# Performance work log

Measured on AMD Instinct MI355X. Metric: run time of the kernel, lower is better.

## Reference

```python
import jax, jax.numpy as jnp
import numpy as np

DIN = 128
HID = 128
B, N = 32, 2048
NEG = 9000000000000000.0


def setup_inputs() -> dict:
    key = jax.random.key(0)
    ks = jax.random.split(key, 8)
    x = jax.random.normal(ks[0], (B, N, DIN), dtype=jnp.float32)
    mask = jax.random.randint(ks[1], (B, N, N), 0, 2).astype(jnp.float32)
    s = 1.0 / np.sqrt(DIN)
    Wv = jax.random.uniform(ks[2], (DIN, HID), minval=-s, maxval=s, dtype=jnp.float32)
    bv = jax.random.uniform(ks[3], (HID,), minval=-s, maxval=s, dtype=jnp.float32)
    Wk = jax.random.uniform(ks[4], (DIN, HID), minval=-s, maxval=s, dtype=jnp.float32)
    bk = jax.random.uniform(ks[5], (HID,), minval=-s, maxval=s, dtype=jnp.float32)
    Wq = jax.random.uniform(ks[6], (DIN, HID), minval=-s, maxval=s, dtype=jnp.float32)
    bq = jax.random.uniform(ks[7], (HID,), minval=-s, maxval=s, dtype=jnp.float32)
    return {"x": x, "mask": mask, "Wv": Wv, "bv": bv, "Wk": Wk, "bk": bk, "Wq": Wq, "bq": bq}


def reference(x, mask, Wv, bv, Wk, bk, Wq, bq):
    v = jnp.tanh(x @ Wv + bv)            # [B, N, H]
    q = jnp.tanh(x @ Wq + bq)            # [B, N, H]
    k = jnp.tanh(x @ Wk + bk)            # [B, N, H]
    scores = jnp.einsum('bih,bjh->bij', q, k)  # [B, N, N]
    scores = scores * mask - NEG * (1.0 - mask)
    att = jax.nn.softmax(scores, axis=-1)
    out = jnp.einsum('bij,bjh->bih', att, v)   # [B, N, H]
    return out
```

## Files before the change

kernel.cpp:

```cpp
#include <hip/hip_runtime.h>

#define DIN 128
#define HID 128
#define BB  32
#define NN  2048
#define LOG2E 1.44269504088896340736f
#define PROJ_BLOCKS 1024
#define COMP_BLOCKS 32768

typedef float  f32x4   __attribute__((ext_vector_type(4)));
typedef __bf16 bf16x4v __attribute__((ext_vector_type(4)));
typedef __bf16 bf16x8  __attribute__((ext_vector_type(8)));

__device__ __forceinline__ float tanh_fast(float x) {
  float e = __expf(2.0f * x);
  return 1.0f - 2.0f / (e + 1.0f);
}

__global__ __launch_bounds__(256) void wt_kernel(
    const float* __restrict__ Wq, const float* __restrict__ Wk,
    const float* __restrict__ Wv, __bf16* __restrict__ wt) {
  const float* W = (blockIdx.x == 0) ? Wq : (blockIdx.x == 1) ? Wk : Wv;
  __bf16* dst = wt + blockIdx.x * (DIN * HID);
  int t = threadIdx.x;
#pragma unroll
  for (int c = 0; c < 16; ++c) {
    int o = c * 1024 + t * 4;
    int d = o >> 7, h = o & 127;
    f32x4 v = *(const f32x4*)(W + d * HID + h);
    dst[(h + 0) * DIN + d] = (__bf16)v.x;
    dst[(h + 1) * DIN + d] = (__bf16)v.y;
    dst[(h + 2) * DIN + d] = (__bf16)v.z;
    dst[(h + 3) * DIN + d] = (__bf16)v.w;
  }
}

__global__ __launch_bounds__(256) void proj_kernel(
    const float* __restrict__ x, const __bf16* __restrict__ wt,
    const float* __restrict__ bq, const float* __restrict__ bk,
    const float* __restrict__ bv, const float* __restrict__ mask,
    __bf16* __restrict__ qbf, __bf16* __restrict__ kbf,
    __bf16* __restrict__ vtbf, unsigned short* __restrict__ bits) {
  const int tid = threadIdx.x;

  if (blockIdx.x >= PROJ_BLOCKS) {
    const long cidx = (long)(blockIdx.x - PROJ_BLOCKS) * 256 + tid;
    const int quad = (int)(cidx & 3);
    const int jt = (int)((cidx >> 2) & 31);
    const long grow = cidx >> 7;
    const float* mp = mask + grow * NN + jt * 64 + quad * 4;
    float mb = 0.f;
#pragma unroll
    for (int t = 0; t < 4; ++t) {
      f32x4 mr = *(const f32x4*)(mp + t * 16);
#pragma unroll
      for (int r = 0; r < 4; ++r)
        mb = fmaf(mr[r], (float)(1u << (t * 4 + r)), mb);
    }
    bits[cidx] = (unsigned short)(unsigned)mb;
    return;
  }

  int lane = tid & 63, w = tid >> 6;
  int l15 = lane & 15, quad = lane >> 4;
  long i0 = (long)blockIdx.x * 64;

  bf16x8 bx[4][4];
#pragma unroll
  for (int nt = 0; nt < 4; ++nt) {
    const float* xp = x + (i0 + nt * 16 + l15) * DIN;
#pragma unroll
    for (int ks = 0; ks < 4; ++ks) {
      int d0 = ks * 32 + quad * 8;
      f32x4 a = *(const f32x4*)(xp + d0);
      f32x4 b = *(const f32x4*)(xp + d0 + 4);
      bf16x8 f;
      f[0] = (__bf16)a.x; f[1] = (__bf16)a.y; f[2] = (__bf16)a.z; f[3] = (__bf16)a.w;
      f[4] = (__bf16)b.x; f[5] = (__bf16)b.y; f[6] = (__bf16)b.z; f[7] = (__bf16)b.w;
      bx[nt][ks] = f;
    }
  }

#pragma unroll
  for (int p = 0; p < 2; ++p) {
    const __bf16* wtp = wt + p * DIN * HID;
    const float* bias = (p == 0) ? bq : bk;
    __bf16* outp = (p == 0) ? qbf : kbf;
#pragma unroll
    for (int nt = 0; nt < 8; ++nt) {
      int h0 = nt * 16 + l15;
      f32x4 acc = {0.f, 0.f, 0.f, 0.f};
#pragma unroll
      for (int ks = 0; ks < 4; ++ks) {
        bf16x8 wf = *(const bf16x8*)(wtp + (long)h0 * DIN + ks * 32 + quad * 8);
        acc = __builtin_amdgcn_mfma_f32_16x16x32_bf16(bx[w][ks], wf, acc, 0, 0, 0);
      }
      float bcol = bias[h0];
      long rowb = i0 + w * 16 + quad * 4;
#pragma unroll
      for (int r = 0; r < 4; ++r) {
        float val = tanh_fast(acc[r] + bcol);
        if (p == 0) val *= LOG2E;
        outp[(rowb + r) * HID + h0] = (__bf16)val;
      }
    }
  }

  {
    const __bf16* wtp = wt + 2 * DIN * HID;
    long bb = i0 >> 11;
    int nloc = (int)(i0 & 2047);
    long vbase = bb * (long)HID * NN;
#pragma unroll
    for (int s = 0; s < 2; ++s) {
      int hb = w * 32 + s * 16;
      bf16x8 af[4];
#pragma unroll
      for (int ks = 0; ks < 4; ++ks)
        af[ks] = *(const bf16x8*)(wtp + (long)(hb + l15) * DIN + ks * 32 + quad * 8);
      float bvr[4];
#pragma unroll
      for (int r = 0; r < 4; ++r) bvr[r] = bv[hb + quad * 4 + r];
#pragma unroll
      for (int nt = 0; nt < 4; ++nt) {
        f32x4 acc = {0.f, 0.f, 0.f, 0.f};
#pragma unroll
        for (int ks = 0; ks < 4; ++ks)
          acc = __builtin_amdgcn_mfma_f32_16x16x32_bf16(af[ks], bx[nt][ks], acc, 0, 0, 0);
        int hrow = hb + quad * 4;
        int ncol = nloc + nt * 16 + l15;
#pragma unroll
        for (int r = 0; r < 4; ++r) {
          float val = tanh_fast(acc[r] + bvr[r]);
          vtbf[vbase + (long)(hrow + r) * NN + ncol] = (__bf16)val;
        }
      }
    }
  }
}

#define KSTR 136
#define VSTR 72
#define PSTR 72

__global__ __launch_bounds__(512, 4) void attn_kernel(
    const __bf16* __restrict__ qbf, const __bf16* __restrict__ kbf,
    const __bf16* __restrict__ vtbf, const unsigned short* __restrict__ bits,
    float* __restrict__ out) {
  __shared__ __bf16 Ks[64 * KSTR];
  __shared__ __bf16 Vts[128 * VSTR];
  __shared__ __bf16 Pl[8 * 16 * PSTR];

  const int tid = threadIdx.x;
  const int lane = tid & 63, w = tid >> 6;
  const int l15 = lane & 15, quad = lane >> 4;
  const int bid = blockIdx.x;
  const int vb = (bid >> 3) | ((bid & 7) << 6);
  const int b = vb >> 4;
  const int i0 = (vb & 15) * 128;
  const long kvbase = (long)b * NN * HID;

  bf16x8 qf[4];
  {
    const __bf16* qp =
        qbf + kvbase + (long)(i0 + w * 16 + l15) * HID + quad * 8;
#pragma unroll
    for (int ks = 0; ks < 4; ++ks) qf[ks] = *(const bf16x8*)(qp + ks * 32);
  }

  const int krow = tid >> 4, kcol = (tid & 15) * 8;
  const int vrow = tid >> 3, vcol = (tid & 7) * 8;
  const __bf16* kg = kbf + kvbase + (long)krow * HID + kcol;
  const __bf16* vg = vtbf + (long)b * HID * NN + (long)vrow * NN + vcol;
  __bf16* ksd0 = Ks + krow * KSTR + kcol;
  __bf16* ksd1 = Ks + (krow + 32) * KSTR + kcol;
  __bf16* vsd0 = Vts + vrow * VSTR + vcol;
  __bf16* vsd1 = Vts + (vrow + 64) * VSTR + vcol;
  const unsigned short* bitp =
      bits + ((long)b * NN + (i0 + w * 16 + l15)) * 128 + quad;
  __bf16* Pw = Pl + w * 16 * PSTR;

  f32x4 O[8];
#pragma unroll
  for (int i = 0; i < 8; ++i) O[i] = (f32x4){0.f, 0.f, 0.f, 0.f};
  float mrow = -1e30f, lrow = 0.0f;

  bf16x8 kr0 = *(const bf16x8*)(kg);
  bf16x8 kr1 = *(const bf16x8*)(kg + 32 * HID);
  bf16x8 vr0 = *(const bf16x8*)(vg);
  bf16x8 vr1 = *(const bf16x8*)(vg + (long)64 * NN);
  unsigned mcur = bitp[0];
  *(bf16x8*)ksd0 = kr0; *(bf16x8*)ksd1 = kr1;
  *(bf16x8*)vsd0 = vr0; *(bf16x8*)vsd1 = vr1;
  __syncthreads();

#pragma unroll 1
  for (int jt = 0; jt < 32; ++jt) {
    const int jn = (jt < 31) ? jt + 1 : 31;
    {
      const __bf16* kgn = kg + (long)jn * 64 * HID;
      kr0 = *(const bf16x8*)(kgn);
      kr1 = *(const bf16x8*)(kgn + 32 * HID);
      const __bf16* vgn = vg + jn * 64;
      vr0 = *(const bf16x8*)(vgn);
      vr1 = *(const bf16x8*)(vgn + (long)64 * NN);
    }
    const unsigned mnext = bitp[jn * 4];

    f32x4 S[4];
#pragma unroll
    for (int t = 0; t < 4; ++t) {
      f32x4 acc = {0.f, 0.f, 0.f, 0.f};
      const __bf16* kp = Ks + (t * 16 + l15) * KSTR + quad * 8;
#pragma unroll
      for (int ks = 0; ks < 4; ++ks) {
        bf16x8 kf = *(const bf16x8*)(kp + ks * 32);
        acc = __builtin_amdgcn_mfma_f32_16x16x32_bf16(kf, qf[ks], acc, 0, 0, 0);
      }
      S[t] = acc;
    }

    float tmx = -1e30f;
#pragma unroll
    for (int t = 0; t < 4; ++t)
#pragma unroll
      for (int r = 0; r < 4; ++r) {
        float s = ((mcur >> (t * 4 + r)) & 1u) ? S[t][r] : -1e30f;
        S[t][r] = s;
        tmx = fmaxf(tmx, s);
      }
    tmx = fmaxf(tmx, __shfl_xor(tmx, 16));
    tmx = fmaxf(tmx, __shfl_xor(tmx, 32));
    const float mnew = fmaxf(mrow, tmx);
    const float alpha = exp2f(mrow - mnew);
    float rs = 0.0f;
#pragma unroll
    for (int t = 0; t < 4; ++t) {
      bf16x4v pb;
#pragma unroll
      for (int r = 0; r < 4; ++r) {
        float p = exp2f(S[t][r] - mnew);
        rs += p;
        pb[r] = (__bf16)p;
      }
      *(bf16x4v*)(Pw + l15 * PSTR + t * 16 + quad * 4) = pb;
    }
    rs += __shfl_xor(rs, 16);
    rs += __shfl_xor(rs, 32);
    lrow = lrow * alpha + rs;
    mrow = mnew;

    float ar[4];
#pragma unroll
    for (int r = 0; r < 4; ++r) ar[r] = __shfl(alpha, (quad << 2) + r);
#pragma unroll
    for (int nt = 0; nt < 8; ++nt)
#pragma unroll
      for (int r = 0; r < 4; ++r) O[nt][r] *= ar[r];

    const bf16x8 pf0 = *(const bf16x8*)(Pw + l15 * PSTR + quad * 8);
    const bf16x8 pf1 = *(const bf16x8*)(Pw + l15 * PSTR + 32 + quad * 8);

#pragma unroll
    for (int nt = 0; nt < 8; ++nt) {
      const __bf16* vp = Vts + (nt * 16 + l15) * VSTR + quad * 8;
      bf16x8 vf0 = *(const bf16x8*)(vp);
      bf16x8 vf1 = *(const bf16x8*)(vp + 32);
      O[nt] = __builtin_amdgcn_mfma_f32_16x16x32_bf16(pf0, vf0, O[nt], 0, 0, 0);
      O[nt] = __builtin_amdgcn_mfma_f32_16x16x32_bf16(pf1, vf1, O[nt], 0, 0, 0);
    }

    __syncthreads();
    *(bf16x8*)ksd0 = kr0; *(bf16x8*)ksd1 = kr1;
    *(bf16x8*)vsd0 = vr0; *(bf16x8*)vsd1 = vr1;
    mcur = mnext;
    __syncthreads();
  }

  const float inv = 1.0f / lrow;
  float il[4];
#pragma unroll
  for (int r = 0; r < 4; ++r) il[r] = __shfl(inv, (quad << 2) + r);
  const long rowb = (long)b * NN + i0 + w * 16 + quad * 4;
#pragma unroll
  for (int r = 0; r < 4; ++r) {
    float* op = out + (rowb + r) * HID;
#pragma unroll
    for (int nt = 0; nt < 8; ++nt) op[nt * 16 + l15] = O[nt][r] * il[r];
  }
}

extern "C" void kernel_launch(void* const* d_in, const int* in_sizes, int n_in,
                              void* d_out, int out_size, void* d_ws, size_t ws_size,
                              hipStream_t stream) {
  const float* x    = (const float*)d_in[0];
  const float* mask = (const float*)d_in[1];
  const float* Wv   = (const float*)d_in[2];
  const float* bv   = (const float*)d_in[3];
  const float* Wk   = (const float*)d_in[4];
  const float* bk   = (const float*)d_in[5];
  const float* Wq   = (const float*)d_in[6];
  const float* bq   = (const float*)d_in[7];
  float* out = (float*)d_out;

  __bf16* ws = (__bf16*)d_ws;
  __bf16* wt   = ws;
  __bf16* qbf  = ws + 3 * DIN * HID;
  __bf16* kbf  = qbf + (long)BB * NN * HID;
  __bf16* vtbf = kbf + (long)BB * NN * HID;
  unsigned short* bits = (unsigned short*)(vtbf + (long)BB * NN * HID);

  wt_kernel<<<3, 256, 0, stream>>>(Wq, Wk, Wv, wt);
  proj_kernel<<<PROJ_BLOCKS + COMP_BLOCKS, 256, 0, stream>>>(
      x, wt, bq, bk, bv, mask, qbf, kbf, vtbf, bits);
  attn_kernel<<<512, 512, 0, stream>>>(qbf, kbf, vtbf, bits, out);
}
```

Before: 912.9 us.

## Interleave mask compression with projection blocks and transpose mask-bit layout

Each mask-compression thread now handles a full 64-column tile, producing four 16-bit words packed into one 64-bit store, so the grid shrinks from 33792 to 9216 blocks. Projection blocks are interleaved with mask blocks (every ninth block) so the memory-bound mask pass overlaps with the compute-bound projection. The bit array is relaid out as [b][jt][row][quad], which makes the attention kernel's per-tile mask reads contiguous across rows. The cost is larger per-thread loads, with each thread reading 256 contiguous bytes, which could make mask reads less coalesced.

```diff
diff --git a/kernel.cpp b/kernel.cpp
--- a/kernel.cpp
+++ b/kernel.cpp
@@ -5,8 +5,6 @@
 #define BB  32
 #define NN  2048
 #define LOG2E 1.44269504088896340736f
-#define PROJ_BLOCKS 1024
-#define COMP_BLOCKS 32768
 
 typedef float  f32x4   __attribute__((ext_vector_type(4)));
 typedef __bf16 bf16x4v __attribute__((ext_vector_type(4)));
@@ -43,27 +41,34 @@
     __bf16* __restrict__ vtbf, unsigned short* __restrict__ bits) {
   const int tid = threadIdx.x;
 
-  if (blockIdx.x >= PROJ_BLOCKS) {
-    const long cidx = (long)(blockIdx.x - PROJ_BLOCKS) * 256 + tid;
-    const int quad = (int)(cidx & 3);
-    const int jt = (int)((cidx >> 2) & 31);
-    const long grow = cidx >> 7;
-    const float* mp = mask + grow * NN + jt * 64 + quad * 4;
-    float mb = 0.f;
-#pragma unroll
-    for (int t = 0; t < 4; ++t) {
-      f32x4 mr = *(const f32x4*)(mp + t * 16);
+  if (blockIdx.x % 9 != 8) {
+    const long cb = (long)blockIdx.x - blockIdx.x / 9;
+    const long gid = cb * 256 + tid;
+    const int jt = (int)(gid & 31);
+    const long rg = gid >> 5;
+    const float* mp = mask + rg * NN + jt * 64;
+    float acc[4] = {0.f, 0.f, 0.f, 0.f};
+#pragma unroll
+    for (int j = 0; j < 16; ++j) {
+      f32x4 v = *(const f32x4*)(mp + j * 4);
+      const int q = j & 3, t = j >> 2;
 #pragma unroll
       for (int r = 0; r < 4; ++r)
-        mb = fmaf(mr[r], (float)(1u << (t * 4 + r)), mb);
-    }
-    bits[cidx] = (unsigned short)(unsigned)mb;
+        acc[q] = fmaf(v[r], (float)(1u << (t * 4 + r)), acc[q]);
+    }
+    unsigned long long pack = 0;
+#pragma unroll
+    for (int q = 0; q < 4; ++q)
+      pack |= (unsigned long long)(unsigned short)(unsigned)acc[q] << (16 * q);
+    const long b_ = rg >> 11, row = rg & 2047;
+    ((unsigned long long*)bits)[b_ * 65536 + (long)jt * 2048 + row] = pack;
     return;
   }
 
+  const long pid = blockIdx.x / 9;
   int lane = tid & 63, w = tid >> 6;
   int l15 = lane & 15, quad = lane >> 4;
-  long i0 = (long)blockIdx.x * 64;
+  long i0 = pid * 64;
 
   bf16x8 bx[4][4];
 #pragma unroll
@@ -177,7 +182,7 @@
   __bf16* vsd0 = Vts + vrow * VSTR + vcol;
   __bf16* vsd1 = Vts + (vrow + 64) * VSTR + vcol;
   const unsigned short* bitp =
-      bits + ((long)b * NN + (i0 + w * 16 + l15)) * 128 + quad;
+      bits + (long)b * 262144 + (long)(i0 + w * 16 + l15) * 4 + quad;
   __bf16* Pw = Pl + w * 16 * PSTR;
 
   f32x4 O[8];
@@ -205,7 +210,7 @@
       vr0 = *(const bf16x8*)(vgn);
       vr1 = *(const bf16x8*)(vgn + (long)64 * NN);
     }
-    const unsigned mnext = bitp[jn * 4];
+    const unsigned mnext = bitp[(long)jn * 8192];
 
     f32x4 S[4];
 #pragma unroll
@@ -311,7 +316,7 @@
   unsigned short* bits = (unsigned short*)(vtbf + (long)BB * NN * HID);
 
   wt_kernel<<<3, 256, 0, stream>>>(Wq, Wk, Wv, wt);
-  proj_kernel<<<PROJ_BLOCKS + COMP_BLOCKS, 256, 0, stream>>>(
+  proj_kernel<<<9216, 256, 0, stream>>>(
       x, wt, bq, bk, bv, mask, qbf, kbf, vtbf, bits);
   attn_kernel<<<512, 512, 0, stream>>>(qbf, kbf, vtbf, bits, out);
 }
```

After: 940.7 us. +3.0%, slower.
